# Kernel tuning notes

Measured on AMD Instinct MI355X. Metric: run time of the kernel, lower is better.

Reference implementation:

```python
import jax, jax.numpy as jnp
import numpy as np

H = 512  # hidden_dim
T = 12   # pred_seq_len
D_OUT = 2


def setup_inputs() -> dict:
    key = jax.random.key(0)
    ks = jax.random.split(key, 13)
    s = lambda fan: 1.0 / np.sqrt(fan)
    return {
        "z":    jax.random.normal(ks[0], (4096, 128), jnp.float32),
        "x":    jax.random.normal(ks[1], (4096, 128), jnp.float32),
        "x_0":  jax.random.normal(ks[2], (4096, 4), jnp.float32),
        "W_ia": jax.random.normal(ks[3], (2, 4), jnp.float32) * s(4),
        "b_ia": jax.random.normal(ks[4], (2,), jnp.float32) * s(4),
        "W_h0": jax.random.normal(ks[5], (H, 256), jnp.float32) * s(256),
        "b_h0": jax.random.normal(ks[6], (H,), jnp.float32) * s(256),
        "W_ih": jax.random.normal(ks[7], (3 * H, 258), jnp.float32) * s(H),
        "b_ih": jax.random.normal(ks[8], (3 * H,), jnp.float32) * s(H),
        "W_hh": jax.random.normal(ks[9], (3 * H, H), jnp.float32) * s(H),
        "b_hh": jax.random.normal(ks[10], (3 * H,), jnp.float32) * s(H),
        "W_out": jax.random.normal(ks[11], (D_OUT, H), jnp.float32) * s(H),
        "b_out": jax.random.normal(ks[12], (D_OUT,), jnp.float32) * s(H),
        "num_samples": 1,
    }


def _gru_cell(inp, h, W_ih, b_ih, W_hh, b_hh):
    # torch.nn.GRUCell math
    gi = inp @ W_ih.T + b_ih  # [N, 3H]
    gh = h @ W_hh.T + b_hh    # [N, 3H]
    gi_r, gi_z, gi_n = jnp.split(gi, 3, axis=-1)
    gh_r, gh_z, gh_n = jnp.split(gh, 3, axis=-1)
    r = jax.nn.sigmoid(gi_r + gh_r)
    u = jax.nn.sigmoid(gi_z + gh_z)
    n = jnp.tanh(gi_n + r * gh_n)
    return (1.0 - u) * n + u * h


def reference(z, x, x_0, W_ia, b_ia, W_h0, b_h0, W_ih, b_ih, W_hh, b_hh, W_out, b_out, num_samples):
    zx = jnp.concatenate([z, x], axis=-1)          # [N, 256]
    h0 = zx @ W_h0.T + b_h0                        # [N, H]
    a0 = x_0 @ W_ia.T + b_ia                       # [N, 2] initial action

    def step(carry, _):
        h, x_t = carry
        inp = jnp.concatenate([zx, x_t], axis=-1)  # [N, 258]
        h_new = _gru_cell(inp, h, W_ih, b_ih, W_hh, b_hh)
        out = h_new @ W_out.T + b_out              # [N, 2]
        # sample_traj with 'mse' loss: deterministic mean
        return (h_new, out), out

    (_, _), outs = jax.lax.scan(step, (h0, a0), None, length=T)  # outs: [T, N, 2]
    N = z.shape[0]
    outs = outs.reshape(T, num_samples, N // num_samples, D_OUT)
    return jnp.transpose(outs, (1, 2, 0, 3))       # [S, B, T, 2]
```

## Files before the change

### kernel.cpp

```cpp
#include <hip/hip_runtime.h>
#include <cstdint>
#include <cstddef>


typedef __attribute__((ext_vector_type(8))) _Float16 f16x8;
typedef __attribute__((ext_vector_type(4))) float floatx4;

__device__ unsigned g_cnt[8 * 64];
__device__ unsigned g_gbar[16 * 64];

__device__ __align__(256) _Float16 g_h[12][16 * 16 * 256 * 32];
__device__ __align__(256) float    g_P[12][16 * 16 * 512];

__device__ __forceinline__ float sigm_f(float v) { return 1.0f / (1.0f + __expf(-v)); }
__device__ __forceinline__ float tanh_f(float v) { return 2.0f / (1.0f + __expf(-2.0f * v)) - 1.0f; }

__device__ __forceinline__ void async16(void* lds, const void* g) {
    __builtin_amdgcn_global_load_lds(
        (const __attribute__((address_space(1))) void*)g,
        (__attribute__((address_space(3))) void*)lds, 16, 0, 0);
}

__device__ __forceinline__ void group_barrier16(unsigned gidx) {
    asm volatile("s_waitcnt vmcnt(0)" ::: "memory");
    __syncthreads();
    if (threadIdx.x == 0) {
        unsigned* ctr = &g_gbar[gidx * 64];
        unsigned t = __hip_atomic_fetch_add(ctr, 1u, __ATOMIC_RELAXED,
                                            __HIP_MEMORY_SCOPE_AGENT);
        unsigned target = (t & ~15u) + 16u;
        while (__hip_atomic_load(ctr, __ATOMIC_RELAXED,
                                 __HIP_MEMORY_SCOPE_AGENT) < target)
            __builtin_amdgcn_s_sleep(1);
    }
    __syncthreads();
}

__global__ __launch_bounds__(256) void k0_prep(
    const float* __restrict__ z, const float* __restrict__ x,
    const float* __restrict__ x0, const float* __restrict__ W_ia,
    const float* __restrict__ b_ia, const float* __restrict__ W_ih,
    const float* __restrict__ W_hh, const float* __restrict__ W_h0,
    const float* __restrict__ W_out, const float* __restrict__ b_hh,
    _Float16* __restrict__ zx16, _Float16* __restrict__ wcat16,
    _Float16* __restrict__ whh16, float* __restrict__ pk, float* __restrict__ xbuf)
{
    const int ZX = 4096 * 256, WC = 2048 * 256, WH = 1536 * 512, PKN = 512, XB = 4096 * 2;
    const int total = ZX + WC + WH + PKN + XB;
    for (int idx = blockIdx.x * 256 + threadIdx.x; idx < total; idx += gridDim.x * 256) {
        if (idx < ZX) {
            int i = idx >> 8, k = idx & 255;
            float v = (k < 128) ? z[i * 128 + k] : x[i * 128 + (k - 128)];
            zx16[idx] = (_Float16)v;
        } else if (idx < ZX + WC) {
            int j = idx - ZX;
            int n = j >> 8, k = j & 255;
            float v = (n < 512) ? W_h0[n * 256 + k] : W_ih[(n - 512) * 258 + k];
            wcat16[j] = (_Float16)v;
        } else if (idx < ZX + WC + WH) {
            int j = idx - ZX - WC;
            whh16[j] = (_Float16)W_hh[j];
        } else if (idx < ZX + WC + WH + PKN) {
            int jc = idx - ZX - WC - WH;
            float* o = pk + jc * 12;
            o[0] = W_ih[jc * 258 + 256];          o[1] = W_ih[jc * 258 + 257];
            o[2] = W_ih[(512 + jc) * 258 + 256];  o[3] = W_ih[(512 + jc) * 258 + 257];
            o[4] = W_ih[(1024 + jc) * 258 + 256]; o[5] = W_ih[(1024 + jc) * 258 + 257];
            o[6] = b_hh[jc]; o[7] = b_hh[512 + jc]; o[8] = b_hh[1024 + jc];
            o[9] = W_out[jc]; o[10] = W_out[512 + jc]; o[11] = 0.f;
        } else {
            int j = idx - ZX - WC - WH - PKN;
            int i = j >> 1, d = j & 1;
            float s = b_ia[d];
            #pragma unroll
            for (int k2 = 0; k2 < 4; k2++) s += x0[i * 4 + k2] * W_ia[d * 4 + k2];
            xbuf[j] = s;
        }
    }
}

__global__ __launch_bounds__(512, 2) void k2_fused(
    const _Float16* __restrict__ zx16, const _Float16* __restrict__ wcat16,
    const _Float16* __restrict__ whh16, const float* __restrict__ pk,
    const float* __restrict__ xbuf, const float* __restrict__ b_h0,
    const float* __restrict__ b_ih, float* __restrict__ dout,
    const float* __restrict__ b_out)
{
    extern __shared__ __align__(16) char smem[];
    const uint32_t BOFF = 0, HST = 98304, XSO = 114688, DOUT = 116736,
                   DUM = 141312, SLO = 142336;
    const int tid = threadIdx.x;
    float* xs = (float*)(smem + XSO);
    float* douts = (float*)(smem + DOUT);

    unsigned xcc;
    asm volatile("s_getreg_b32 %0, hwreg(HW_REG_XCC_ID)" : "=s"(xcc));
    xcc &= 7u;
    if (tid == 0) {
        unsigned s = __hip_atomic_fetch_add(&g_cnt[xcc * 64], 1u, __ATOMIC_RELAXED,
                                            __HIP_MEMORY_SCOPE_AGENT) & 31u;
        *(unsigned*)(smem + SLO) = s;
    }
    __syncthreads();
    const unsigned slot = *(volatile unsigned*)(smem + SLO);
    const int shalf = slot >> 4, cgrp = slot & 15;
    const unsigned gidx = xcc * 2 + shalf;
    const int M0g = (int)gidx * 256;
    const int jc0 = cgrp * 32;

    const int wv = tid >> 6, lane = tid & 63;
    const int l15 = lane & 15, q2 = lane >> 4;

    if (wv == 0) {
        const char* wb = (const char*)&g_h[0][0] + (size_t)gidx * 262144 +
                         (size_t)cgrp * 16384 + (size_t)lane * 128;
        async16(smem + DUM, wb);
        async16(smem + DUM, wb + 8192);
    }
    if (wv == 1) {
        const char* wp = (const char*)&g_P[0][0] +
                         ((size_t)gidx * 8192 + (size_t)cgrp * 512) * 4 +
                         (size_t)(lane & 15) * 128;
        async16(smem + DUM, wp);
    }

    #pragma unroll
    for (int j2 = 0; j2 < 8; j2++) {
        int p = j2 * 8 + wv;
        int r0 = p * 2;
        int r = r0 + (lane >> 5);
        int s = lane & 31;
        int n = (r < 96) ? (512 + (r >> 5) * 512 + jc0 + (r & 31))
                         : (jc0 + (r - 96));
        const _Float16* src = wcat16 + (size_t)n * 256 + ((s ^ (r & 15)) << 3);
        async16(smem + (uint32_t)r0 * 512, src);
    }

    float4 p0v[2], p1v[2], p2v[2]; float wo0[2], wo1[2];
    float bih[3][2], bh0[2];
    #pragma unroll
    for (int jt = 0; jt < 2; jt++) {
        int jc = jc0 + jt * 16 + l15;
        const float4* pkp = (const float4*)(pk + (size_t)jc * 12);
        p0v[jt] = pkp[0]; p1v[jt] = pkp[1]; p2v[jt] = pkp[2];
        wo0[jt] = p2v[jt].y; wo1[jt] = p2v[jt].z;
        bh0[jt] = b_h0[jc];
        #pragma unroll
        for (int g = 0; g < 3; g++) bih[g][jt] = b_ih[g * 512 + jc];
    }
    float bo = b_out[lane & 1];

    uint32_t bbase[6];
    #pragma unroll
    for (int g = 0; g < 3; g++)
        #pragma unroll
        for (int jt = 0; jt < 2; jt++) {
            int r = g * 32 + jt * 16 + l15;
            bbase[g * 2 + jt] = BOFF + (uint32_t)r * 1024 +
                                ((uint32_t)(q2 ^ (r & 3)) << 4) +
                                ((uint32_t)((r >> 2) & 3) << 6);
        }
    uint32_t pb[8];
    #pragma unroll
    for (int sl = 0; sl < 8; sl++) {
        int r = (sl < 6) ? ((sl >> 1) * 32 + (sl & 1) * 16 + l15)
                         : (96 + (sl - 6) * 16 + l15);
        pb[sl] = BOFF + (uint32_t)r * 512 +
                 ((uint32_t)(q2 ^ (r & 3)) << 4) +
                 ((uint32_t)((r >> 2) & 3) << 6);
    }
    __syncthreads();

    const char* zp0 = (const char*)zx16 +
        ((size_t)(M0g + (wv * 2 + 0) * 16 + l15) * 256) * 2 + (size_t)q2 * 16;
    const char* zp1 = (const char*)zx16 +
        ((size_t)(M0g + (wv * 2 + 1) * 16 + l15) * 256) * 2 + (size_t)q2 * 16;
    floatx4 accP[2][8];
    #pragma unroll
    for (int mt = 0; mt < 2; mt++)
        #pragma unroll
        for (int sl = 0; sl < 8; sl++) accP[mt][sl] = (floatx4){0.f, 0.f, 0.f, 0.f};
    {
        f16x8 aq[4][2];
        #define ALOADZ(S, KS) do { \
            aq[S][0] = *(const f16x8*)(zp0 + (KS) * 64); \
            aq[S][1] = *(const f16x8*)(zp1 + (KS) * 64); \
        } while (0)
        ALOADZ(0, 0); ALOADZ(1, 1); ALOADZ(2, 2);
        #pragma unroll
        for (int ks = 0; ks < 8; ks++) {
            if (ks < 5) { ALOADZ((ks + 3) & 3, ks + 3); }
            f16x8 a0 = aq[ks & 3][0];
            f16x8 a1 = aq[ks & 3][1];
            const uint32_t kadd = (uint32_t)((ks >> 2) << 8);
            const uint32_t kxor = (uint32_t)((ks & 3) << 6);
            #pragma unroll
            for (int sl = 0; sl < 8; sl++) {
                f16x8 b = *(const f16x8*)(smem + ((pb[sl] + kadd) ^ kxor));
                accP[0][sl] = __builtin_amdgcn_mfma_f32_16x16x32_f16(a0, b, accP[0][sl], 0, 0, 0);
                accP[1][sl] = __builtin_amdgcn_mfma_f32_16x16x32_f16(a1, b, accP[1][sl], 0, 0, 0);
            }
        }
        #undef ALOADZ
    }

    float gi[2][3][2][4];
    #pragma unroll
    for (int mt = 0; mt < 2; mt++)
        #pragma unroll
        for (int g = 0; g < 3; g++)
            #pragma unroll
            for (int jt = 0; jt < 2; jt++)
                #pragma unroll
                for (int reg = 0; reg < 4; reg++)
                    gi[mt][g][jt][reg] = accP[mt][g * 2 + jt][reg] + bih[g][jt];
    #pragma unroll
    for (int mt = 0; mt < 2; mt++)
        #pragma unroll
        for (int jt = 0; jt < 2; jt++)
            #pragma unroll
            for (int reg = 0; reg < 4; reg++) {
                int rl = (wv * 2 + mt) * 16 + q2 * 4 + reg;
                float v = accP[mt][6 + jt][reg] + bh0[jt];
                *(_Float16*)(smem + HST + (uint32_t)(rl * 64 + (jt * 16 + l15) * 2)) = (_Float16)v;
            }
    __syncthreads();

    #pragma unroll
    for (int j = 0; j < 12; j++) {
        int r = j * 8 + wv;
        int n = (r >> 5) * 512 + jc0 + (r & 31);
        const _Float16* src = whh16 + (size_t)n * 512 + ((lane ^ (r & 15)) << 3);
        async16(smem + BOFF + (uint32_t)r * 1024, src);
    }
    {
        int row = tid >> 1, half = tid & 1;
        const char* sl = smem + HST + (uint32_t)(row * 64 + half * 32);
        char* gd = (char*)&g_h[0][0] + (size_t)gidx * 262144 + (size_t)cgrp * 16384 +
                   (size_t)row * 64 + (size_t)half * 32;
        *(f16x8*)gd = *(const f16x8*)sl;
        *(f16x8*)(gd + 16) = *(const f16x8*)(sl + 16);
    }
    group_barrier16(gidx);

    #pragma unroll 1
    for (int t = 0; t < 12; t++) {
        if (t < 11 && wv == 0) {
            const char* wb = (const char*)&g_h[t + 1][0] + (size_t)gidx * 262144 +
                             (size_t)cgrp * 16384 + (size_t)lane * 128;
            async16(smem + DUM, wb);
            async16(smem + DUM, wb + 8192);
        }
        if (wv == 1) {
            const char* wp = (const char*)&g_P[t][0] +
                             ((size_t)gidx * 8192 + (size_t)cgrp * 512) * 4 +
                             (size_t)(lane & 15) * 128;
            async16(smem + DUM, wp);
        }

        const char* hb = (const char*)&g_h[t][0] + (size_t)gidx * 262144 + (size_t)q2 * 16;
        const char* rp0 = hb + (size_t)((wv * 2 + 0) * 16 + l15) * 64;
        const char* rp1 = hb + (size_t)((wv * 2 + 1) * 16 + l15) * 64;
        floatx4 acc[2][3][2];
        #pragma unroll
        for (int mt = 0; mt < 2; mt++)
            #pragma unroll
            for (int g = 0; g < 3; g++)
                #pragma unroll
                for (int jt = 0; jt < 2; jt++)
                    acc[mt][g][jt] = (floatx4){0.f, 0.f, 0.f, 0.f};

        f16x8 aq[4][2];
        #define ALOAD(S, KS) do { \
            aq[S][0] = *(const f16x8*)(rp0 + (size_t)(KS) * 16384); \
            aq[S][1] = *(const f16x8*)(rp1 + (size_t)(KS) * 16384); \
        } while (0)
        ALOAD(0, 0); ALOAD(1, 1); ALOAD(2, 2);

        float pv[16];
        if (t > 0) {
            const float* pbase = &g_P[t - 1][0] + (size_t)gidx * 8192 +
                                 (size_t)(wv * 32 + (lane >> 1)) * 2 + (size_t)(lane & 1);
            #pragma unroll
            for (int c = 0; c < 16; c++) pv[c] = pbase[c * 512];
        }

        #pragma unroll
        for (int ks = 0; ks < 16; ks++) {
            if (ks < 13) { ALOAD((ks + 3) & 3, ks + 3); }
            f16x8 a0 = aq[ks & 3][0];
            f16x8 a1 = aq[ks & 3][1];
            const uint32_t kadd = (uint32_t)((ks >> 2) << 8);
            const uint32_t kxor = (uint32_t)((ks & 3) << 6);
            #pragma unroll
            for (int g = 0; g < 3; g++)
                #pragma unroll
                for (int jt = 0; jt < 2; jt++) {
                    f16x8 b = *(const f16x8*)(smem + ((bbase[g * 2 + jt] + kadd) ^ kxor));
                    acc[0][g][jt] = __builtin_amdgcn_mfma_f32_16x16x32_f16(a0, b, acc[0][g][jt], 0, 0, 0);
                    acc[1][g][jt] = __builtin_amdgcn_mfma_f32_16x16x32_f16(a1, b, acc[1][g][jt], 0, 0, 0);
                }
        }
        #undef ALOAD

        {
            float v;
            if (t == 0) {
                v = xbuf[(size_t)(M0g + wv * 32 + (lane >> 1)) * 2 + (lane & 1)];
            } else {
                v = bo;
                #pragma unroll
                for (int c = 0; c < 16; c++) v += pv[c];
                douts[wv * 768 + (t - 1) * 64 + lane] = v;
            }
            xs[wv * 64 + lane] = v;
        }

        #pragma unroll
        for (int mt = 0; mt < 2; mt++) {
            float po[4][2];
            #pragma unroll
            for (int reg = 0; reg < 4; reg++) { po[reg][0] = 0.f; po[reg][1] = 0.f; }
            #pragma unroll
            for (int jt = 0; jt < 2; jt++) {
                #pragma unroll
                for (int reg = 0; reg < 4; reg++) {
                    int local = mt * 16 + q2 * 4 + reg;
                    int rl = wv * 32 + local;
                    float2 xv = *(const float2*)(smem + XSO + (uint32_t)((wv * 64 + local * 2) * 4));
                    _Float16* hp = (_Float16*)(smem + HST + (uint32_t)(rl * 64 + (jt * 16 + l15) * 2));
                    float hold = (float)hp[0];
                    float r  = sigm_f(gi[mt][0][jt][reg] + p0v[jt].x * xv.x + p0v[jt].y * xv.y + acc[mt][0][jt][reg] + p1v[jt].z);
                    float u  = sigm_f(gi[mt][1][jt][reg] + p0v[jt].z * xv.x + p0v[jt].w * xv.y + acc[mt][1][jt][reg] + p1v[jt].w);
                    float nn = tanh_f(gi[mt][2][jt][reg] + p1v[jt].x * xv.x + p1v[jt].y * xv.y + r * (acc[mt][2][jt][reg] + p2v[jt].x));
                    float hn = (1.f - u) * nn + u * hold;
                    hp[0] = (_Float16)hn;
                    po[reg][0] += hn * wo0[jt];
                    po[reg][1] += hn * wo1[jt];
                }
            }
            #pragma unroll
            for (int m = 1; m < 16; m <<= 1)
                #pragma unroll
                for (int reg = 0; reg < 4; reg++) {
                    po[reg][0] += __shfl_xor(po[reg][0], m);
                    po[reg][1] += __shfl_xor(po[reg][1], m);
                }
            if (l15 == 0) {
                #pragma unroll
                for (int reg = 0; reg < 4; reg++) {
                    int local = mt * 16 + q2 * 4 + reg;
                    float* pp = &g_P[t][0] + (size_t)gidx * 8192 + (size_t)cgrp * 512 +
                                (size_t)(wv * 32 + local) * 2;
                    *(float2*)pp = make_float2(po[reg][0], po[reg][1]);
                }
            }
        }

        if (t < 11) {
            int rloc = wv * 32 + (lane >> 1);
            int half = lane & 1;
            const char* sl = smem + HST + (uint32_t)(rloc * 64 + half * 32);
            char* gd = (char*)&g_h[t + 1][0] + (size_t)gidx * 262144 +
                       (size_t)cgrp * 16384 + (size_t)rloc * 64 + (size_t)half * 32;
            *(f16x8*)gd = *(const f16x8*)sl;
            *(f16x8*)(gd + 16) = *(const f16x8*)(sl + 16);
        }
        group_barrier16(gidx);
    }

    if (cgrp == 0) {
        const float* pbase = &g_P[11][0] + (size_t)gidx * 8192 +
                             (size_t)(wv * 32 + (lane >> 1)) * 2 + (size_t)(lane & 1);
        float v = bo;
        #pragma unroll
        for (int c = 0; c < 16; c++) v += pbase[c * 512];
        douts[wv * 768 + 11 * 64 + lane] = v;
        size_t i = (size_t)(M0g + wv * 32 + (lane >> 1));
        int d = lane & 1;
        #pragma unroll
        for (int t = 0; t < 12; t++)
            dout[(i * 12 + t) * 2 + d] = douts[wv * 768 + t * 64 + lane];
    }
}

extern "C" void kernel_launch(void* const* d_in, const int* in_sizes, int n_in,
                              void* d_out, int out_size, void* d_ws, size_t ws_size,
                              hipStream_t stream)
{
    const float* z     = (const float*)d_in[0];
    const float* x     = (const float*)d_in[1];
    const float* x0    = (const float*)d_in[2];
    const float* W_ia  = (const float*)d_in[3];
    const float* b_ia  = (const float*)d_in[4];
    const float* W_h0  = (const float*)d_in[5];
    const float* b_h0  = (const float*)d_in[6];
    const float* W_ih  = (const float*)d_in[7];
    const float* b_ih  = (const float*)d_in[8];
    const float* W_hh  = (const float*)d_in[9];
    const float* b_hh  = (const float*)d_in[10];
    const float* W_out = (const float*)d_in[11];
    const float* b_out = (const float*)d_in[12];
    float* dout = (float*)d_out;

    char* ws = (char*)d_ws;
    _Float16* zx16   = (_Float16*)(ws + 20971520);
    _Float16* wcat16 = (_Float16*)(ws + 23068672);
    _Float16* whh16  = (_Float16*)(ws + 24117248);
    float*    pk     = (float*)(ws + 25690112);
    float*    xbuf   = (float*)(ws + 25714688);

    static bool s_attr_done = false;
    if (!s_attr_done) {
        hipFuncSetAttribute((const void*)k2_fused,
                            hipFuncAttributeMaxDynamicSharedMemorySize, 142400);
        s_attr_done = true;
    }

    k0_prep<<<2048, 256, 0, stream>>>(z, x, x0, W_ia, b_ia, W_ih, W_hh, W_h0,
                                      W_out, b_hh, zx16, wcat16, whh16, pk, xbuf);
    k2_fused<<<256, 512, 142400, stream>>>(zx16, wcat16, whh16, pk, xbuf,
                                           b_h0, b_ih, dout, b_out);
}
```

Measured before the change: 268.2 us.

## Fold output projection into recurrent weights and recompute outputs locally from full hidden state

```diff
diff --git a/kernel.cpp b/kernel.cpp
--- a/kernel.cpp
+++ b/kernel.cpp
@@ -5,12 +5,12 @@
 
 typedef __attribute__((ext_vector_type(8))) _Float16 f16x8;
 typedef __attribute__((ext_vector_type(4))) float floatx4;
+typedef _Float16 h2 __attribute__((ext_vector_type(2)));
 
 __device__ unsigned g_cnt[8 * 64];
 __device__ unsigned g_gbar[16 * 64];
 
-__device__ __align__(256) _Float16 g_h[12][16 * 16 * 256 * 32];
-__device__ __align__(256) float    g_P[12][16 * 16 * 512];
+__device__ __align__(256) _Float16 g_h[13][16 * 16 * 256 * 32];
 
 __device__ __forceinline__ float sigm_f(float v) { return 1.0f / (1.0f + __expf(-v)); }
 __device__ __forceinline__ float tanh_f(float v) { return 2.0f / (1.0f + __expf(-2.0f * v)) - 1.0f; }
@@ -19,6 +19,27 @@
     __builtin_amdgcn_global_load_lds(
         (const __attribute__((address_space(1))) void*)g,
         (__attribute__((address_space(3))) void*)lds, 16, 0, 0);
+}
+
+union H8 { f16x8 v; h2 p[4]; };
+
+__device__ __forceinline__ void dot8(float& acc0, float& acc1,
+                                     f16x8 a, f16x8 w0, f16x8 w1) {
+#if __has_builtin(__builtin_amdgcn_fdot2)
+    H8 ha{a}, hw0{w0}, hw1{w1};
+    #pragma unroll
+    for (int p = 0; p < 4; p++) {
+        acc0 = __builtin_amdgcn_fdot2(ha.p[p], hw0.p[p], acc0, false);
+        acc1 = __builtin_amdgcn_fdot2(ha.p[p], hw1.p[p], acc1, false);
+    }
+#else
+    #pragma unroll
+    for (int e = 0; e < 8; e++) {
+        float av = (float)a[e];
+        acc0 += av * (float)w0[e];
+        acc1 += av * (float)w1[e];
+    }
+#endif
 }
 
 __device__ __forceinline__ void group_barrier16(unsigned gidx) {
@@ -42,11 +63,14 @@
     const float* __restrict__ b_ia, const float* __restrict__ W_ih,
     const float* __restrict__ W_hh, const float* __restrict__ W_h0,
     const float* __restrict__ W_out, const float* __restrict__ b_hh,
+    const float* __restrict__ b_out,
     _Float16* __restrict__ zx16, _Float16* __restrict__ wcat16,
-    _Float16* __restrict__ whh16, float* __restrict__ pk, float* __restrict__ xbuf)
+    _Float16* __restrict__ whh16, _Float16* __restrict__ wo16,
+    float* __restrict__ pk, float* __restrict__ xbuf)
 {
-    const int ZX = 4096 * 256, WC = 2048 * 256, WH = 1536 * 512, PKN = 512, XB = 4096 * 2;
-    const int total = ZX + WC + WH + PKN + XB;
+    const int ZX = 4096 * 256, WC = 2048 * 256, WH = 1536 * 512, PKN = 512,
+              XB = 4096 * 2, WO = 1024;
+    const int total = ZX + WC + WH + PKN + XB + WO;
     for (int idx = blockIdx.x * 256 + threadIdx.x; idx < total; idx += gridDim.x * 256) {
         if (idx < ZX) {
             int i = idx >> 8, k = idx & 255;
@@ -59,22 +83,32 @@
             wcat16[j] = (_Float16)v;
         } else if (idx < ZX + WC + WH) {
             int j = idx - ZX - WC;
-            whh16[j] = (_Float16)W_hh[j];
+            int n = j >> 9, k = j & 511;
+            float v = W_hh[j];
+            if (n < 1024)
+                v += W_ih[n * 258 + 256] * W_out[k] +
+                     W_ih[n * 258 + 257] * W_out[512 + k];
+            whh16[j] = (_Float16)v;
         } else if (idx < ZX + WC + WH + PKN) {
             int jc = idx - ZX - WC - WH;
             float* o = pk + jc * 12;
             o[0] = W_ih[jc * 258 + 256];          o[1] = W_ih[jc * 258 + 257];
             o[2] = W_ih[(512 + jc) * 258 + 256];  o[3] = W_ih[(512 + jc) * 258 + 257];
             o[4] = W_ih[(1024 + jc) * 258 + 256]; o[5] = W_ih[(1024 + jc) * 258 + 257];
-            o[6] = b_hh[jc]; o[7] = b_hh[512 + jc]; o[8] = b_hh[1024 + jc];
+            o[6] = b_hh[jc] + o[0] * b_out[0] + o[1] * b_out[1];
+            o[7] = b_hh[512 + jc] + o[2] * b_out[0] + o[3] * b_out[1];
+            o[8] = b_hh[1024 + jc];
             o[9] = W_out[jc]; o[10] = W_out[512 + jc]; o[11] = 0.f;
-        } else {
+        } else if (idx < ZX + WC + WH + PKN + XB) {
             int j = idx - ZX - WC - WH - PKN;
             int i = j >> 1, d = j & 1;
             float s = b_ia[d];
             #pragma unroll
             for (int k2 = 0; k2 < 4; k2++) s += x0[i * 4 + k2] * W_ia[d * 4 + k2];
             xbuf[j] = s;
+        } else {
+            int j = idx - ZX - WC - WH - PKN - XB;
+            wo16[j] = (_Float16)W_out[j];
         }
     }
 }
@@ -83,14 +117,13 @@
     const _Float16* __restrict__ zx16, const _Float16* __restrict__ wcat16,
     const _Float16* __restrict__ whh16, const float* __restrict__ pk,
     const float* __restrict__ xbuf, const float* __restrict__ b_h0,
-    const float* __restrict__ b_ih, float* __restrict__ dout,
-    const float* __restrict__ b_out)
+    const float* __restrict__ b_ih, const _Float16* __restrict__ wo16g,
+    const float* __restrict__ b_out, float* __restrict__ dout)
 {
     extern __shared__ __align__(16) char smem[];
     const uint32_t BOFF = 0, HST = 98304, XSO = 114688, DOUT = 116736,
-                   DUM = 141312, SLO = 142336;
+                   DUM = 141312, SLO = 142336, WOUT = 142400, XDO = 144448;
     const int tid = threadIdx.x;
-    float* xs = (float*)(smem + XSO);
     float* douts = (float*)(smem + DOUT);
 
     unsigned xcc;
@@ -101,6 +134,10 @@
                                             __HIP_MEMORY_SCOPE_AGENT) & 31u;
         *(unsigned*)(smem + SLO) = s;
     }
+    if (tid < 128) {
+        f16x8 v = *(const f16x8*)(wo16g + tid * 8);
+        *(f16x8*)(smem + WOUT + (uint32_t)tid * 16) = v;
+    }
     __syncthreads();
     const unsigned slot = *(volatile unsigned*)(smem + SLO);
     const int shalf = slot >> 4, cgrp = slot & 15;
@@ -116,12 +153,6 @@
                          (size_t)cgrp * 16384 + (size_t)lane * 128;
         async16(smem + DUM, wb);
         async16(smem + DUM, wb + 8192);
-    }
-    if (wv == 1) {
-        const char* wp = (const char*)&g_P[0][0] +
-                         ((size_t)gidx * 8192 + (size_t)cgrp * 512) * 4 +
-                         (size_t)(lane & 15) * 128;
-        async16(smem + DUM, wp);
     }
 
     #pragma unroll
@@ -136,19 +167,18 @@
         async16(smem + (uint32_t)r0 * 512, src);
     }
 
-    float4 p0v[2], p1v[2], p2v[2]; float wo0[2], wo1[2];
+    float4 p0v[2], p1v[2], p2v[2];
     float bih[3][2], bh0[2];
     #pragma unroll
     for (int jt = 0; jt < 2; jt++) {
         int jc = jc0 + jt * 16 + l15;
         const float4* pkp = (const float4*)(pk + (size_t)jc * 12);
         p0v[jt] = pkp[0]; p1v[jt] = pkp[1]; p2v[jt] = pkp[2];
-        wo0[jt] = p2v[jt].y; wo1[jt] = p2v[jt].z;
         bh0[jt] = b_h0[jc];
         #pragma unroll
         for (int g = 0; g < 3; g++) bih[g][jt] = b_ih[g * 512 + jc];
     }
-    float bo = b_out[lane & 1];
+    const float bo0 = b_out[0], bo1 = b_out[1];
 
     uint32_t bbase[6];
     #pragma unroll
@@ -245,18 +275,12 @@
 
     #pragma unroll 1
     for (int t = 0; t < 12; t++) {
-        if (t < 11 && wv == 0) {
+        if (wv == 0) {
             const char* wb = (const char*)&g_h[t + 1][0] + (size_t)gidx * 262144 +
                              (size_t)cgrp * 16384 + (size_t)lane * 128;
             async16(smem + DUM, wb);
             async16(smem + DUM, wb + 8192);
         }
-        if (wv == 1) {
-            const char* wp = (const char*)&g_P[t][0] +
-                             ((size_t)gidx * 8192 + (size_t)cgrp * 512) * 4 +
-                             (size_t)(lane & 15) * 128;
-            async16(smem + DUM, wp);
-        }
 
         const char* hb = (const char*)&g_h[t][0] + (size_t)gidx * 262144 + (size_t)q2 * 16;
         const char* rp0 = hb + (size_t)((wv * 2 + 0) * 16 + l15) * 64;
@@ -269,6 +293,7 @@
                 #pragma unroll
                 for (int jt = 0; jt < 2; jt++)
                     acc[mt][g][jt] = (floatx4){0.f, 0.f, 0.f, 0.f};
+        float xacc[2][2] = {{0.f, 0.f}, {0.f, 0.f}};
 
         f16x8 aq[4][2];
         #define ALOAD(S, KS) do { \
@@ -276,15 +301,6 @@
             aq[S][1] = *(const f16x8*)(rp1 + (size_t)(KS) * 16384); \
         } while (0)
         ALOAD(0, 0); ALOAD(1, 1); ALOAD(2, 2);
-
-        float pv[16];
-        if (t > 0) {
-            const float* pbase = &g_P[t - 1][0] + (size_t)gidx * 8192 +
-                                 (size_t)(wv * 32 + (lane >> 1)) * 2 + (size_t)(lane & 1);
-            #pragma unroll
-            for (int c = 0; c < 16; c++) pv[c] = pbase[c * 512];
-        }
-
         #pragma unroll
         for (int ks = 0; ks < 16; ks++) {
             if (ks < 13) { ALOAD((ks + 3) & 3, ks + 3); }
@@ -300,69 +316,75 @@
                     acc[0][g][jt] = __builtin_amdgcn_mfma_f32_16x16x32_f16(a0, b, acc[0][g][jt], 0, 0, 0);
                     acc[1][g][jt] = __builtin_amdgcn_mfma_f32_16x16x32_f16(a1, b, acc[1][g][jt], 0, 0, 0);
                 }
+            f16x8 w0v = *(const f16x8*)(smem + WOUT + (uint32_t)(ks * 64 + q2 * 16));
+            f16x8 w1v = *(const f16x8*)(smem + WOUT + 1024u + (uint32_t)(ks * 64 + q2 * 16));
+            dot8(xacc[0][0], xacc[0][1], a0, w0v, w1v);
+            dot8(xacc[1][0], xacc[1][1], a1, w0v, w1v);
         }
         #undef ALOAD
 
-        {
-            float v;
-            if (t == 0) {
-                v = xbuf[(size_t)(M0g + wv * 32 + (lane >> 1)) * 2 + (lane & 1)];
-            } else {
-                v = bo;
-                #pragma unroll
-                for (int c = 0; c < 16; c++) v += pv[c];
-                douts[wv * 768 + (t - 1) * 64 + lane] = v;
-            }
-            xs[wv * 64 + lane] = v;
+        #pragma unroll
+        for (int mt = 0; mt < 2; mt++)
+            #pragma unroll
+            for (int d = 0; d < 2; d++) {
+                xacc[mt][d] += __shfl_xor(xacc[mt][d], 16);
+                xacc[mt][d] += __shfl_xor(xacc[mt][d], 32);
+            }
+        float xc[2][2];
+        xc[0][0] = xacc[0][0] + bo0; xc[0][1] = xacc[0][1] + bo1;
+        xc[1][0] = xacc[1][0] + bo0; xc[1][1] = xacc[1][1] + bo1;
+        if (q2 == 0) {
+            #pragma unroll
+            for (int mt = 0; mt < 2; mt++) {
+                int local = mt * 16 + l15;
+                if (t == 0) {
+                    float a00 = xbuf[(size_t)(M0g + wv * 32 + local) * 2 + 0];
+                    float a01 = xbuf[(size_t)(M0g + wv * 32 + local) * 2 + 1];
+                    ((float2*)(smem + XSO))[wv * 32 + local] = make_float2(a00, a01);
+                    ((float2*)(smem + XDO))[wv * 32 + local] =
+                        make_float2(a00 - xc[mt][0], a01 - xc[mt][1]);
+                } else {
+                    ((float2*)(smem + XSO))[wv * 32 + local] = make_float2(xc[mt][0], xc[mt][1]);
+                    if (cgrp == 0)
+                        ((float2*)douts)[wv * 384 + (t - 1) * 32 + local] =
+                            make_float2(xc[mt][0], xc[mt][1]);
+                }
+            }
         }
 
         #pragma unroll
         for (int mt = 0; mt < 2; mt++) {
-            float po[4][2];
-            #pragma unroll
-            for (int reg = 0; reg < 4; reg++) { po[reg][0] = 0.f; po[reg][1] = 0.f; }
             #pragma unroll
             for (int jt = 0; jt < 2; jt++) {
                 #pragma unroll
                 for (int reg = 0; reg < 4; reg++) {
                     int local = mt * 16 + q2 * 4 + reg;
                     int rl = wv * 32 + local;
-                    float2 xv = *(const float2*)(smem + XSO + (uint32_t)((wv * 64 + local * 2) * 4));
+                    float2 xv = ((const float2*)(smem + XSO))[wv * 32 + local];
                     _Float16* hp = (_Float16*)(smem + HST + (uint32_t)(rl * 64 + (jt * 16 + l15) * 2));
                     float hold = (float)hp[0];
-                    float r  = sigm_f(gi[mt][0][jt][reg] + p0v[jt].x * xv.x + p0v[jt].y * xv.y + acc[mt][0][jt][reg] + p1v[jt].z);
-                    float u  = sigm_f(gi[mt][1][jt][reg] + p0v[jt].z * xv.x + p0v[jt].w * xv.y + acc[mt][1][jt][reg] + p1v[jt].w);
-                    float nn = tanh_f(gi[mt][2][jt][reg] + p1v[jt].x * xv.x + p1v[jt].y * xv.y + r * (acc[mt][2][jt][reg] + p2v[jt].x));
+                    float rpre = gi[mt][0][jt][reg] + acc[mt][0][jt][reg] + p1v[jt].z;
+                    float upre = gi[mt][1][jt][reg] + acc[mt][1][jt][reg] + p1v[jt].w;
+                    if (t == 0) {
+                        float2 xdv = ((const float2*)(smem + XDO))[wv * 32 + local];
+                        rpre += p0v[jt].x * xdv.x + p0v[jt].y * xdv.y;
+                        upre += p0v[jt].z * xdv.x + p0v[jt].w * xdv.y;
+                    }
+                    float r = sigm_f(rpre);
+                    float u = sigm_f(upre);
+                    float nn = tanh_f(gi[mt][2][jt][reg] + p1v[jt].x * xv.x + p1v[jt].y * xv.y +
+                                      r * (acc[mt][2][jt][reg] + p2v[jt].x));
                     float hn = (1.f - u) * nn + u * hold;
                     hp[0] = (_Float16)hn;
-                    po[reg][0] += hn * wo0[jt];
-                    po[reg][1] += hn * wo1[jt];
                 }
             }
-            #pragma unroll
-            for (int m = 1; m < 16; m <<= 1)
-                #pragma unroll
-                for (int reg = 0; reg < 4; reg++) {
-                    po[reg][0] += __shfl_xor(po[reg][0], m);
-                    po[reg][1] += __shfl_xor(po[reg][1], m);
-                }
-            if (l15 == 0) {
-                #pragma unroll
-                for (int reg = 0; reg < 4; reg++) {
-                    int local = mt * 16 + q2 * 4 + reg;
-                    float* pp = &g_P[t][0] + (size_t)gidx * 8192 + (size_t)cgrp * 512 +
-                                (size_t)(wv * 32 + local) * 2;
-                    *(float2*)pp = make_float2(po[reg][0], po[reg][1]);
-                }
-            }
-        }
-
-        if (t < 11) {
-            int rloc = wv * 32 + (lane >> 1);
-            int half = lane & 1;
-            const char* sl = smem + HST + (uint32_t)(rloc * 64 + half * 32);
+        }
+
+        {
+            int row = tid >> 1, half = tid & 1;
+            const char* sl = smem + HST + (uint32_t)(row * 64 + half * 32);
             char* gd = (char*)&g_h[t + 1][0] + (size_t)gidx * 262144 +
-                       (size_t)cgrp * 16384 + (size_t)rloc * 64 + (size_t)half * 32;
+                       (size_t)cgrp * 16384 + (size_t)row * 64 + (size_t)half * 32;
             *(f16x8*)gd = *(const f16x8*)sl;
             *(f16x8*)(gd + 16) = *(const f16x8*)(sl + 16);
         }
@@ -370,17 +392,39 @@
     }
 
     if (cgrp == 0) {
-        const float* pbase = &g_P[11][0] + (size_t)gidx * 8192 +
-                             (size_t)(wv * 32 + (lane >> 1)) * 2 + (size_t)(lane & 1);
-        float v = bo;
-        #pragma unroll
-        for (int c = 0; c < 16; c++) v += pbase[c * 512];
-        douts[wv * 768 + 11 * 64 + lane] = v;
-        size_t i = (size_t)(M0g + wv * 32 + (lane >> 1));
+        const char* hb = (const char*)&g_h[12][0] + (size_t)gidx * 262144 + (size_t)q2 * 16;
+        const char* rp0 = hb + (size_t)((wv * 2 + 0) * 16 + l15) * 64;
+        const char* rp1 = hb + (size_t)((wv * 2 + 1) * 16 + l15) * 64;
+        float xa[2][2] = {{0.f, 0.f}, {0.f, 0.f}};
+        #pragma unroll
+        for (int ks = 0; ks < 16; ks++) {
+            f16x8 a0 = *(const f16x8*)(rp0 + (size_t)ks * 16384);
+            f16x8 a1 = *(const f16x8*)(rp1 + (size_t)ks * 16384);
+            f16x8 w0v = *(const f16x8*)(smem + WOUT + (uint32_t)(ks * 64 + q2 * 16));
+            f16x8 w1v = *(const f16x8*)(smem + WOUT + 1024u + (uint32_t)(ks * 64 + q2 * 16));
+            dot8(xa[0][0], xa[0][1], a0, w0v, w1v);
+            dot8(xa[1][0], xa[1][1], a1, w0v, w1v);
+        }
+        #pragma unroll
+        for (int mt = 0; mt < 2; mt++)
+            #pragma unroll
+            for (int d = 0; d < 2; d++) {
+                xa[mt][d] += __shfl_xor(xa[mt][d], 16);
+                xa[mt][d] += __shfl_xor(xa[mt][d], 32);
+            }
+        if (q2 == 0) {
+            #pragma unroll
+            for (int mt = 0; mt < 2; mt++) {
+                int local = mt * 16 + l15;
+                ((float2*)douts)[wv * 384 + 11 * 32 + local] =
+                    make_float2(xa[mt][0] + bo0, xa[mt][1] + bo1);
+            }
+        }
+        size_t i = (size_t)M0g + wv * 32 + (lane >> 1);
         int d = lane & 1;
         #pragma unroll
-        for (int t = 0; t < 12; t++)
-            dout[(i * 12 + t) * 2 + d] = douts[wv * 768 + t * 64 + lane];
+        for (int tt = 0; tt < 12; tt++)
+            dout[(i * 12 + tt) * 2 + d] = douts[wv * 768 + tt * 64 + lane];
     }
 }
 
@@ -409,16 +453,18 @@
     _Float16* whh16  = (_Float16*)(ws + 24117248);
     float*    pk     = (float*)(ws + 25690112);
     float*    xbuf   = (float*)(ws + 25714688);
+    _Float16* wo16   = (_Float16*)(ws + 25747456);
 
     static bool s_attr_done = false;
     if (!s_attr_done) {
         hipFuncSetAttribute((const void*)k2_fused,
-                            hipFuncAttributeMaxDynamicSharedMemorySize, 142400);
+                            hipFuncAttributeMaxDynamicSharedMemorySize, 146496);
         s_attr_done = true;
     }
 
     k0_prep<<<2048, 256, 0, stream>>>(z, x, x0, W_ia, b_ia, W_ih, W_hh, W_h0,
-                                      W_out, b_hh, zx16, wcat16, whh16, pk, xbuf);
-    k2_fused<<<256, 512, 142400, stream>>>(zx16, wcat16, whh16, pk, xbuf,
-                                           b_h0, b_ih, dout, b_out);
-}
+                                      W_out, b_hh, b_out,
+                                      zx16, wcat16, whh16, wo16, pk, xbuf);
+    k2_fused<<<256, 512, 146496, stream>>>(zx16, wcat16, whh16, pk, xbuf,
+                                           b_h0, b_ih, wo16, b_out, dout);
+}
```

Measured after the change: 286.5 us. 6.8% more time.

## Fuse fp16 prep kernel into main GRU kernel, converting weights on load

Applied to the files above, without the earlier changes.

```diff
diff --git a/kernel.cpp b/kernel.cpp
--- a/kernel.cpp
+++ b/kernel.cpp
@@ -19,6 +19,16 @@
     __builtin_amdgcn_global_load_lds(
         (const __attribute__((address_space(1))) void*)g,
         (__attribute__((address_space(3))) void*)lds, 16, 0, 0);
+}
+
+__device__ __forceinline__ f16x8 ldzx8(const float* __restrict__ z,
+                                       const float* __restrict__ x,
+                                       int i, int c) {
+    const float* s = (c < 128) ? (z + (size_t)i * 128 + c)
+                               : (x + (size_t)i * 128 + (c - 128));
+    float4 a = ((const float4*)s)[0], b = ((const float4*)s)[1];
+    return (f16x8){(_Float16)a.x, (_Float16)a.y, (_Float16)a.z, (_Float16)a.w,
+                   (_Float16)b.x, (_Float16)b.y, (_Float16)b.z, (_Float16)b.w};
 }
 
 __device__ __forceinline__ void group_barrier16(unsigned gidx) {
@@ -36,55 +46,14 @@
     __syncthreads();
 }
 
-__global__ __launch_bounds__(256) void k0_prep(
+__global__ __launch_bounds__(512, 2) void k_all(
     const float* __restrict__ z, const float* __restrict__ x,
     const float* __restrict__ x0, const float* __restrict__ W_ia,
-    const float* __restrict__ b_ia, const float* __restrict__ W_ih,
-    const float* __restrict__ W_hh, const float* __restrict__ W_h0,
-    const float* __restrict__ W_out, const float* __restrict__ b_hh,
-    _Float16* __restrict__ zx16, _Float16* __restrict__ wcat16,
-    _Float16* __restrict__ whh16, float* __restrict__ pk, float* __restrict__ xbuf)
-{
-    const int ZX = 4096 * 256, WC = 2048 * 256, WH = 1536 * 512, PKN = 512, XB = 4096 * 2;
-    const int total = ZX + WC + WH + PKN + XB;
-    for (int idx = blockIdx.x * 256 + threadIdx.x; idx < total; idx += gridDim.x * 256) {
-        if (idx < ZX) {
-            int i = idx >> 8, k = idx & 255;
-            float v = (k < 128) ? z[i * 128 + k] : x[i * 128 + (k - 128)];
-            zx16[idx] = (_Float16)v;
-        } else if (idx < ZX + WC) {
-            int j = idx - ZX;
-            int n = j >> 8, k = j & 255;
-            float v = (n < 512) ? W_h0[n * 256 + k] : W_ih[(n - 512) * 258 + k];
-            wcat16[j] = (_Float16)v;
-        } else if (idx < ZX + WC + WH) {
-            int j = idx - ZX - WC;
-            whh16[j] = (_Float16)W_hh[j];
-        } else if (idx < ZX + WC + WH + PKN) {
-            int jc = idx - ZX - WC - WH;
-            float* o = pk + jc * 12;
-            o[0] = W_ih[jc * 258 + 256];          o[1] = W_ih[jc * 258 + 257];
-            o[2] = W_ih[(512 + jc) * 258 + 256];  o[3] = W_ih[(512 + jc) * 258 + 257];
-            o[4] = W_ih[(1024 + jc) * 258 + 256]; o[5] = W_ih[(1024 + jc) * 258 + 257];
-            o[6] = b_hh[jc]; o[7] = b_hh[512 + jc]; o[8] = b_hh[1024 + jc];
-            o[9] = W_out[jc]; o[10] = W_out[512 + jc]; o[11] = 0.f;
-        } else {
-            int j = idx - ZX - WC - WH - PKN;
-            int i = j >> 1, d = j & 1;
-            float s = b_ia[d];
-            #pragma unroll
-            for (int k2 = 0; k2 < 4; k2++) s += x0[i * 4 + k2] * W_ia[d * 4 + k2];
-            xbuf[j] = s;
-        }
-    }
-}
-
-__global__ __launch_bounds__(512, 2) void k2_fused(
-    const _Float16* __restrict__ zx16, const _Float16* __restrict__ wcat16,
-    const _Float16* __restrict__ whh16, const float* __restrict__ pk,
-    const float* __restrict__ xbuf, const float* __restrict__ b_h0,
-    const float* __restrict__ b_ih, float* __restrict__ dout,
-    const float* __restrict__ b_out)
+    const float* __restrict__ b_ia, const float* __restrict__ W_h0,
+    const float* __restrict__ b_h0, const float* __restrict__ W_ih,
+    const float* __restrict__ b_ih, const float* __restrict__ W_hh,
+    const float* __restrict__ b_hh, const float* __restrict__ W_out,
+    const float* __restrict__ b_out, float* __restrict__ dout)
 {
     extern __shared__ __align__(16) char smem[];
     const uint32_t BOFF = 0, HST = 98304, XSO = 114688, DOUT = 116736,
@@ -125,15 +94,25 @@
     }
 
     #pragma unroll
-    for (int j2 = 0; j2 < 8; j2++) {
-        int p = j2 * 8 + wv;
-        int r0 = p * 2;
-        int r = r0 + (lane >> 5);
-        int s = lane & 31;
-        int n = (r < 96) ? (512 + (r >> 5) * 512 + jc0 + (r & 31))
-                         : (jc0 + (r - 96));
-        const _Float16* src = wcat16 + (size_t)n * 256 + ((s ^ (r & 15)) << 3);
-        async16(smem + (uint32_t)r0 * 512, src);
+    for (int u = 0; u < 8; u++) {
+        int sl2 = u * 512 + tid;
+        int r = sl2 >> 5, s = sl2 & 31;
+        int c = (s ^ (r & 15)) << 3;
+        f16x8 v;
+        if (r < 96) {
+            int nrow = (r >> 5) * 512 + jc0 + (r & 31);
+            const float2* src = (const float2*)(W_ih + (size_t)nrow * 258 + c);
+            float2 a0 = src[0], a1 = src[1], a2 = src[2], a3 = src[3];
+            v = (f16x8){(_Float16)a0.x, (_Float16)a0.y, (_Float16)a1.x, (_Float16)a1.y,
+                        (_Float16)a2.x, (_Float16)a2.y, (_Float16)a3.x, (_Float16)a3.y};
+        } else {
+            int nrow = jc0 + (r - 96);
+            const float4* src = (const float4*)(W_h0 + (size_t)nrow * 256 + c);
+            float4 a = src[0], b = src[1];
+            v = (f16x8){(_Float16)a.x, (_Float16)a.y, (_Float16)a.z, (_Float16)a.w,
+                        (_Float16)b.x, (_Float16)b.y, (_Float16)b.z, (_Float16)b.w};
+        }
+        *(f16x8*)(smem + (uint32_t)(r * 512 + s * 16)) = v;
     }
 
     float4 p0v[2], p1v[2], p2v[2]; float wo0[2], wo1[2];
@@ -141,14 +120,23 @@
     #pragma unroll
     for (int jt = 0; jt < 2; jt++) {
         int jc = jc0 + jt * 16 + l15;
-        const float4* pkp = (const float4*)(pk + (size_t)jc * 12);
-        p0v[jt] = pkp[0]; p1v[jt] = pkp[1]; p2v[jt] = pkp[2];
+        p0v[jt] = make_float4(W_ih[(size_t)jc * 258 + 256],
+                              W_ih[(size_t)jc * 258 + 257],
+                              W_ih[(size_t)(512 + jc) * 258 + 256],
+                              W_ih[(size_t)(512 + jc) * 258 + 257]);
+        p1v[jt] = make_float4(W_ih[(size_t)(1024 + jc) * 258 + 256],
+                              W_ih[(size_t)(1024 + jc) * 258 + 257],
+                              b_hh[jc], b_hh[512 + jc]);
+        p2v[jt] = make_float4(b_hh[1024 + jc], W_out[jc], W_out[512 + jc], 0.f);
         wo0[jt] = p2v[jt].y; wo1[jt] = p2v[jt].z;
         bh0[jt] = b_h0[jc];
         #pragma unroll
         for (int g = 0; g < 3; g++) bih[g][jt] = b_ih[g * 512 + jc];
     }
-    float bo = b_out[lane & 1];
+    const float bo = b_out[lane & 1];
+    const float bia_d = b_ia[lane & 1];
+    float4 wia_d = make_float4(W_ia[(lane & 1) * 4 + 0], W_ia[(lane & 1) * 4 + 1],
+                               W_ia[(lane & 1) * 4 + 2], W_ia[(lane & 1) * 4 + 3]);
 
     uint32_t bbase[6];
     #pragma unroll
@@ -171,10 +159,8 @@
     }
     __syncthreads();
 
-    const char* zp0 = (const char*)zx16 +
-        ((size_t)(M0g + (wv * 2 + 0) * 16 + l15) * 256) * 2 + (size_t)q2 * 16;
-    const char* zp1 = (const char*)zx16 +
-        ((size_t)(M0g + (wv * 2 + 1) * 16 + l15) * 256) * 2 + (size_t)q2 * 16;
+    const int ia0 = M0g + (wv * 2 + 0) * 16 + l15;
+    const int ia1 = M0g + (wv * 2 + 1) * 16 + l15;
     floatx4 accP[2][8];
     #pragma unroll
     for (int mt = 0; mt < 2; mt++)
@@ -183,8 +169,8 @@
     {
         f16x8 aq[4][2];
         #define ALOADZ(S, KS) do { \
-            aq[S][0] = *(const f16x8*)(zp0 + (KS) * 64); \
-            aq[S][1] = *(const f16x8*)(zp1 + (KS) * 64); \
+            aq[S][0] = ldzx8(z, x, ia0, (KS) * 32 + q2 * 8); \
+            aq[S][1] = ldzx8(z, x, ia1, (KS) * 32 + q2 * 8); \
         } while (0)
         ALOADZ(0, 0); ALOADZ(1, 1); ALOADZ(2, 2);
         #pragma unroll
@@ -227,11 +213,16 @@
     __syncthreads();
 
     #pragma unroll
-    for (int j = 0; j < 12; j++) {
-        int r = j * 8 + wv;
-        int n = (r >> 5) * 512 + jc0 + (r & 31);
-        const _Float16* src = whh16 + (size_t)n * 512 + ((lane ^ (r & 15)) << 3);
-        async16(smem + BOFF + (uint32_t)r * 1024, src);
+    for (int u = 0; u < 12; u++) {
+        int sl2 = u * 512 + tid;
+        int r = sl2 >> 6, l = sl2 & 63;
+        int nrow = (r >> 5) * 512 + jc0 + (r & 31);
+        int c = (l ^ (r & 15)) << 3;
+        const float4* src = (const float4*)(W_hh + (size_t)nrow * 512 + c);
+        float4 a = src[0], b = src[1];
+        f16x8 v = {(_Float16)a.x, (_Float16)a.y, (_Float16)a.z, (_Float16)a.w,
+                   (_Float16)b.x, (_Float16)b.y, (_Float16)b.z, (_Float16)b.w};
+        *(f16x8*)(smem + (uint32_t)(r * 1024 + l * 16)) = v;
     }
     {
         int row = tid >> 1, half = tid & 1;
@@ -306,7 +297,10 @@
         {
             float v;
             if (t == 0) {
-                v = xbuf[(size_t)(M0g + wv * 32 + (lane >> 1)) * 2 + (lane & 1)];
+                int i = M0g + wv * 32 + (lane >> 1);
+                float4 xr = *(const float4*)(x0 + (size_t)i * 4);
+                v = bia_d + xr.x * wia_d.x + xr.y * wia_d.y +
+                            xr.z * wia_d.z + xr.w * wia_d.w;
             } else {
                 v = bo;
                 #pragma unroll
@@ -403,22 +397,14 @@
     const float* b_out = (const float*)d_in[12];
     float* dout = (float*)d_out;
 
-    char* ws = (char*)d_ws;
-    _Float16* zx16   = (_Float16*)(ws + 20971520);
-    _Float16* wcat16 = (_Float16*)(ws + 23068672);
-    _Float16* whh16  = (_Float16*)(ws + 24117248);
-    float*    pk     = (float*)(ws + 25690112);
-    float*    xbuf   = (float*)(ws + 25714688);
-
     static bool s_attr_done = false;
     if (!s_attr_done) {
-        hipFuncSetAttribute((const void*)k2_fused,
+        hipFuncSetAttribute((const void*)k_all,
                             hipFuncAttributeMaxDynamicSharedMemorySize, 142400);
         s_attr_done = true;
     }
 
-    k0_prep<<<2048, 256, 0, stream>>>(z, x, x0, W_ia, b_ia, W_ih, W_hh, W_h0,
-                                      W_out, b_hh, zx16, wcat16, whh16, pk, xbuf);
-    k2_fused<<<256, 512, 142400, stream>>>(zx16, wcat16, whh16, pk, xbuf,
-                                           b_h0, b_ih, dout, b_out);
+    k_all<<<256, 512, 142400, stream>>>(z, x, x0, W_ia, b_ia, W_h0, b_h0,
+                                        W_ih, b_ih, W_hh, b_hh, W_out, b_out,
+                                        dout);
 }
```

Result: no change. 267.8 us (-0.2%).
